# Kernel tuning notes

Hardware: AMD Instinct MI355X
Metric: run time of the kernel (lower is better)

Reference implementation:

```python
import jax, jax.numpy as jnp
import numpy as np

D_MODEL = 2048
NUM_HEADS = 16
HEAD_DIM = 128
ROPE_BASE = 10000.0
NEG_INF = -1e9


def setup_inputs() -> dict:
    key = jax.random.key(0)
    ks = jax.random.split(key, 5)
    B, S = 2, 2048
    hidden_states = jax.random.normal(ks[0], (B, S, D_MODEL), dtype=jnp.float32)
    # additive causal mask: 0 on/below diagonal, large-negative above
    causal = jnp.triu(jnp.full((S, S), NEG_INF, dtype=jnp.float32), k=1)
    attention_mask = jnp.broadcast_to(causal, (B, 1, S, S))
    position_ids = jnp.broadcast_to(jnp.arange(S, dtype=jnp.int32), (B, S))
    scale = 1.0 / np.sqrt(D_MODEL)
    Wq = jax.random.normal(ks[1], (D_MODEL, NUM_HEADS * HEAD_DIM), dtype=jnp.float32) * scale
    Wk = jax.random.normal(ks[2], (D_MODEL, NUM_HEADS * HEAD_DIM), dtype=jnp.float32) * scale
    Wv = jax.random.normal(ks[3], (D_MODEL, NUM_HEADS * HEAD_DIM), dtype=jnp.float32) * scale
    Wo = jax.random.normal(ks[4], (NUM_HEADS * HEAD_DIM, D_MODEL), dtype=jnp.float32) * scale
    return {"hidden_states": hidden_states, "attention_mask": attention_mask,
            "position_ids": position_ids, "Wq": Wq, "Wk": Wk, "Wv": Wv, "Wo": Wo}


def _rope_cos_sin(position_ids):
    # inv_freq: [head_dim/2]
    inv_freq = 1.0 / (ROPE_BASE ** (jnp.arange(0, HEAD_DIM, 2, dtype=jnp.float32) / HEAD_DIM))
    freqs = position_ids.astype(jnp.float32)[..., None] * inv_freq  # [B,S,hd/2]
    emb = jnp.concatenate([freqs, freqs], axis=-1)  # [B,S,hd]
    return jnp.cos(emb), jnp.sin(emb)


def _rotate_half(x):
    x1, x2 = jnp.split(x, 2, axis=-1)
    return jnp.concatenate([-x2, x1], axis=-1)


def reference(hidden_states, attention_mask, position_ids, Wq, Wk, Wv, Wo):
    B, S, _ = hidden_states.shape
    H, Dh = NUM_HEADS, HEAD_DIM
    q = (hidden_states @ Wq).reshape(B, S, H, Dh).transpose(0, 2, 1, 3)  # [B,H,S,Dh]
    k = (hidden_states @ Wk).reshape(B, S, H, Dh).transpose(0, 2, 1, 3)
    v = (hidden_states @ Wv).reshape(B, S, H, Dh).transpose(0, 2, 1, 3)
    cos, sin = _rope_cos_sin(position_ids)  # [B,S,Dh]
    cos = cos[:, None, :, :]  # [B,1,S,Dh]
    sin = sin[:, None, :, :]
    q = q * cos + _rotate_half(q) * sin
    k = k * cos + _rotate_half(k) * sin
    scaling = 1.0 / np.sqrt(Dh)
    scores = jnp.einsum('bhqd,bhkd->bhqk', q, k) * scaling  # [B,H,S,S]
    scores = scores + attention_mask[:, :, :, :S]
    attn = jax.nn.softmax(scores.astype(jnp.float32), axis=-1).astype(q.dtype)
    # dropout p=0.0 / eval mode -> identity
    out = jnp.einsum('bhqk,bhkd->bhqd', attn, v)  # [B,H,S,Dh]
    out = out.transpose(0, 2, 1, 3).reshape(B, S, H * Dh)
    return out @ Wo
```

## Files before the change

### kernel.cpp

```cpp
#include <hip/hip_runtime.h>

typedef __attribute__((ext_vector_type(4))) float f32x4;
typedef __attribute__((ext_vector_type(16))) float f32x16;
typedef __attribute__((ext_vector_type(8))) _Float16 f16x8;
typedef __attribute__((ext_vector_type(4))) _Float16 f16x4;

#define SEQ 2048
#define DM 2048
#define NQKV 6144

__device__ __forceinline__ void gload16(const _Float16* g, _Float16* l) {
  __builtin_amdgcn_global_load_lds(
      (const __attribute__((address_space(1))) void*)g,
      (__attribute__((address_space(3))) void*)l, 16, 0, 0);
}

__global__ __launch_bounds__(256) void cvt_x_kernel(const float* __restrict__ X,
                                                    _Float16* __restrict__ Xb, int n4) {
  int i = blockIdx.x * 256 + threadIdx.x;
  if (i < n4) {
    const float4 v = ((const float4*)X)[i];
    f16x4 o;
    o.x = (_Float16)v.x; o.y = (_Float16)v.y; o.z = (_Float16)v.z; o.w = (_Float16)v.w;
    ((f16x4*)Xb)[i] = o;
  }
}

__global__ __launch_bounds__(256) void wtrans_all_kernel(const float* __restrict__ Wq,
                                                         const float* __restrict__ Wk,
                                                         const float* __restrict__ Wv,
                                                         const float* __restrict__ Wo,
                                                         _Float16* __restrict__ Wqkvt,
                                                         _Float16* __restrict__ Wot) {
  __shared__ float tile[64][65];
  const int z = blockIdx.z;
  const float* W = (z == 0) ? Wq : (z == 1) ? Wk : (z == 2) ? Wv : Wo;
  _Float16* Wt = (z < 3) ? (Wqkvt + (size_t)z * 2048 * 2048) : Wot;
  const int n0 = blockIdx.x * 64, k0 = blockIdx.y * 64;
  const int tx = threadIdx.x & 15, ty = threadIdx.x >> 4;
#pragma unroll
  for (int i = 0; i < 4; ++i) {
    const int r = ty + i * 16;
    const float4 v = *(const float4*)&W[(size_t)(k0 + r) * 2048 + n0 + tx * 4];
    tile[r][tx * 4] = v.x; tile[r][tx * 4 + 1] = v.y;
    tile[r][tx * 4 + 2] = v.z; tile[r][tx * 4 + 3] = v.w;
  }
  __syncthreads();
  const int r = threadIdx.x >> 2, u = threadIdx.x & 3;
  _Float16 o[16];
#pragma unroll
  for (int i = 0; i < 16; ++i) o[i] = (_Float16)tile[u * 16 + i][r];
  _Float16* dst = &Wt[(size_t)(n0 + r) * 2048 + k0 + u * 16];
  *(f16x8*)&dst[0] = *(f16x8*)&o[0];
  *(f16x8*)&dst[8] = *(f16x8*)&o[8];
}

__global__ __launch_bounds__(256) void rope_table_kernel(float* __restrict__ ct,
                                                         float* __restrict__ st) {
  int i = blockIdx.x * 256 + threadIdx.x;
  int pos = i >> 6, f = i & 63;
  float inv = powf(10000.0f, -(float)f / 64.0f);
  float ang = (float)pos * inv;
  ct[i] = cosf(ang);
  st[i] = sinf(ang);
}

#define BARX()                                                          \
  do { __builtin_amdgcn_sched_barrier(0); __builtin_amdgcn_s_barrier(); \
       __builtin_amdgcn_sched_barrier(0); } while (0)
#define LGKM0X()                                                        \
  do { asm volatile("s_waitcnt lgkmcnt(0)" ::: "memory");               \
       __builtin_amdgcn_sched_barrier(0); } while (0)

template <int MODE>
__global__ __launch_bounds__(512, 2) void gemm8n_kernel(
    const _Float16* __restrict__ A, const _Float16* __restrict__ Bt,
    float* __restrict__ Cout, int M, int N, int K,
    const int* __restrict__ pos_ids, const float* __restrict__ ct,
    const float* __restrict__ st, _Float16* __restrict__ Qo,
    _Float16* __restrict__ Ko, _Float16* __restrict__ Vo) {
  __shared__ __align__(16) char smem[147456];
  _Float16* As = (_Float16*)smem;
  _Float16* Bs = (_Float16*)(smem + 98304);
  const int nwg = gridDim.x * gridDim.y;
  const int orig = blockIdx.y * gridDim.x + blockIdx.x;
  const int id = (orig & 7) * (nwg >> 3) + (orig >> 3);
  const int bx = id % gridDim.x, by = id / gridDim.x;
  const int bm = by * 256, bn = bx * 128;
  const int t = threadIdx.x, lane = t & 63, w = t >> 6;
  const int wm = w >> 2, wn = w & 3;
  const int rl = lane & 15, lr4 = lane >> 4;
  const int NKT = K >> 6;

  const int srow = t >> 3;
  const int scol = ((t & 7) ^ (srow & 7)) << 3;
  const _Float16* pA = A + (size_t)(bm + srow) * K + scol;
  const _Float16* pB = Bt + (size_t)(bn + srow) * K + scol;
  _Float16* lA = As + t * 8;
  _Float16* lB = Bs + t * 8;
  const size_t rowK64 = (size_t)64 * K;

#define STA(H, KT, SLOT)                                                   \
  { const size_t _g = (size_t)((H) * 128) * K + (size_t)(KT) * 64;         \
    gload16(pA + _g, lA + (SLOT) * 16384 + (H) * 8192);                    \
    gload16(pA + _g + rowK64, lA + (SLOT) * 16384 + (H) * 8192 + 4096); }
#define STB(KT, SLOT)                                                      \
  { const size_t _g = (size_t)(KT) * 64;                                   \
    gload16(pB + _g, lB + (SLOT) * 8192);                                  \
    gload16(pB + _g + rowK64, lB + (SLOT) * 8192 + 4096); }

  const int sw0 = (lr4 ^ (rl & 7)) << 3;
  const int sw1 = ((4 + lr4) ^ (rl & 7)) << 3;
  const int aoff = (wm * 64 + rl) * 64;
  const int boff = (wn * 32 + rl) * 64;

  f16x8 a_[4][2], b_[2][2];
  f32x4 acc[2][4][2];
#pragma unroll
  for (int qm = 0; qm < 2; ++qm)
#pragma unroll
    for (int mf = 0; mf < 4; ++mf)
#pragma unroll
      for (int nf = 0; nf < 2; ++nf) acc[qm][mf][nf] = (f32x4)0.0f;

#define LOAD_A(H, SLOT)                                                 \
  { const _Float16* _p = As + (SLOT) * 16384 + (H) * 8192 + aoff;       \
    _Pragma("unroll") for (int mf = 0; mf < 4; ++mf) {                  \
      a_[mf][0] = *(const f16x8*)&_p[mf * 1024 + sw0];                  \
      a_[mf][1] = *(const f16x8*)&_p[mf * 1024 + sw1]; } }
#define LOAD_B(SLOT)                                                    \
  { const _Float16* _p = Bs + (SLOT) * 8192 + boff;                     \
    _Pragma("unroll") for (int nf = 0; nf < 2; ++nf) {                  \
      b_[nf][0] = *(const f16x8*)&_p[nf * 1024 + sw0];                  \
      b_[nf][1] = *(const f16x8*)&_p[nf * 1024 + sw1]; } }
#define MFMA_Q(QM)                                                      \
  __builtin_amdgcn_s_setprio(1);                                        \
  _Pragma("unroll") for (int mf = 0; mf < 4; ++mf)                      \
    _Pragma("unroll") for (int nf = 0; nf < 2; ++nf) {                  \
      acc[QM][mf][nf] = __builtin_amdgcn_mfma_f32_16x16x32_f16(         \
          a_[mf][0], b_[nf][0], acc[QM][mf][nf], 0, 0, 0);              \
      acc[QM][mf][nf] = __builtin_amdgcn_mfma_f32_16x16x32_f16(         \
          a_[mf][1], b_[nf][1], acc[QM][mf][nf], 0, 0, 0); }            \
  __builtin_amdgcn_s_setprio(0);
#define VM6() asm volatile("s_waitcnt vmcnt(6)" ::: "memory")
#define VM0() asm volatile("s_waitcnt vmcnt(0)" ::: "memory")

  STA(0, 0, 0); STB(0, 0); STA(1, 0, 0);
  STA(0, 1, 1); STB(1, 1); STA(1, 1, 1);
  VM6();
  BARX();

  for (int jb = 0; jb + 4 < NKT; jb += 3) {
    LOAD_A(0, 0); LOAD_B(0); STA(0, jb + 2, 2); STB(jb + 2, 2);
    BARX(); LGKM0X(); MFMA_Q(0); BARX();
    LOAD_A(1, 0); STA(1, jb + 2, 2);
    VM6(); BARX(); LGKM0X(); MFMA_Q(1); BARX();
    LOAD_A(0, 1); LOAD_B(1); STA(0, jb + 3, 0); STB(jb + 3, 0);
    BARX(); LGKM0X(); MFMA_Q(0); BARX();
    LOAD_A(1, 1); STA(1, jb + 3, 0);
    VM6(); BARX(); LGKM0X(); MFMA_Q(1); BARX();
    LOAD_A(0, 2); LOAD_B(2); STA(0, jb + 4, 1); STB(jb + 4, 1);
    BARX(); LGKM0X(); MFMA_Q(0); BARX();
    LOAD_A(1, 2); STA(1, jb + 4, 1);
    VM6(); BARX(); LGKM0X(); MFMA_Q(1); BARX();
  }
  {
    LOAD_A(0, 0); LOAD_B(0);
    BARX(); LGKM0X(); MFMA_Q(0); BARX();
    LOAD_A(1, 0);
    VM0();
    BARX(); LGKM0X(); MFMA_Q(1); BARX();
    LOAD_A(0, 1); LOAD_B(1);
    BARX(); LGKM0X(); MFMA_Q(0); BARX();
    LOAD_A(1, 1);
    BARX(); LGKM0X(); MFMA_Q(1);
  }

  if (MODE == 0) {
#pragma unroll
    for (int qm = 0; qm < 2; ++qm)
#pragma unroll
      for (int mf = 0; mf < 4; ++mf)
#pragma unroll
        for (int nf = 0; nf < 2; ++nf) {
          const int col = bn + wn * 32 + nf * 16 + rl;
#pragma unroll
          for (int ri = 0; ri < 4; ++ri) {
            const int row = bm + qm * 128 + wm * 64 + mf * 16 + lr4 * 4 + ri;
            Cout[(size_t)row * N + col] = acc[qm][mf][nf][ri];
          }
        }
  } else {
    const int ttype = bx >> 4;
    const int hh = bx & 15;
    if (ttype == 2) {
#pragma unroll
      for (int qm = 0; qm < 2; ++qm)
#pragma unroll
        for (int mf = 0; mf < 4; ++mf)
#pragma unroll
          for (int nf = 0; nf < 2; ++nf) {
            const int d = wn * 32 + nf * 16 + rl;
            const int s0 = bm + qm * 128 + wm * 64 + mf * 16 + lr4 * 4;
            const int bb = s0 >> 11, ss = s0 & 2047;
            f16x4 v4;
#pragma unroll
            for (int ri = 0; ri < 4; ++ri) v4[ri] = (_Float16)acc[qm][mf][nf][ri];
            *(f16x4*)&Vo[((size_t)(bb * 16 + hh) * 128 + d) * SEQ + ss] = v4;
          }
    } else {
      float* cl = (float*)smem;
      LGKM0X();
      BARX();
#pragma unroll
      for (int qm = 0; qm < 2; ++qm)
#pragma unroll
        for (int mf = 0; mf < 4; ++mf)
#pragma unroll
          for (int nf = 0; nf < 2; ++nf) {
            const int col = wn * 32 + nf * 16 + rl;
            const int r0 = qm * 128 + wm * 64 + mf * 16 + lr4 * 4;
#pragma unroll
            for (int ri = 0; ri < 4; ++ri) cl[(r0 + ri) * 130 + col] = acc[qm][mf][nf][ri];
          }
      BARX();
      const int row = t >> 1, pb = (t & 1) * 32;
      const int rg = bm + row;
      const int bb = rg >> 11, ss = rg & 2047;
      const int pos = pos_ids[rg];
      const float* cp = ct + pos * 64 + pb;
      const float* sp = st + pos * 64 + pb;
      _Float16* dst = (ttype ? Ko : Qo) + ((size_t)(bb * 16 + hh) * SEQ + ss) * 128;
      const float qs = ttype ? 1.0f : 0.08838834764831845f;
      const float* crow = cl + row * 130;
      _Float16 o1[32], o2[32];
#pragma unroll
      for (int i = 0; i < 32; ++i) {
        const float x1 = crow[pb + i], x2 = crow[pb + 64 + i];
        const float c = cp[i], s = sp[i];
        o1[i] = (_Float16)((x1 * c - x2 * s) * qs);
        o2[i] = (_Float16)((x2 * c + x1 * s) * qs);
      }
#pragma unroll
      for (int i = 0; i < 4; ++i) {
        *(f16x8*)&dst[pb + i * 8] = *(f16x8*)&o1[i * 8];
        *(f16x8*)&dst[pb + 64 + i * 8] = *(f16x8*)&o2[i * 8];
      }
    }
  }
#undef STA
#undef STB
#undef LOAD_A
#undef LOAD_B
#undef MFMA_Q
#undef VM6
#undef VM0
}

__global__ __launch_bounds__(512) void attn_kernel(const _Float16* __restrict__ Q,
                                                   const _Float16* __restrict__ K,
                                                   const _Float16* __restrict__ Vt,
                                                   _Float16* __restrict__ O) {
  __shared__ __align__(16) _Float16 Ks[2][128 * 128];
  __shared__ __align__(16) _Float16 Vs[2][128 * 128];
  __shared__ __align__(16) _Float16 Ps[128 * 128];
  const int bh = blockIdx.x;
  const int pair = blockIdx.y;
  const int b = bh >> 4, h = bh & 15;
  const int t = threadIdx.x, lane = t & 63, w = t >> 6;
  const int rowgrp = w & 3, kh = w >> 2;
  const int l31 = lane & 31, l5 = lane >> 5;
  const _Float16* Qb = Q + (size_t)bh * SEQ * 128;
  const _Float16* Kb = K + (size_t)bh * SEQ * 128;
  const _Float16* Vb = Vt + (size_t)bh * 128 * SEQ;

  f16x8 onef;
#pragma unroll
  for (int i = 0; i < 8; ++i) onef[i] = (_Float16)1.0f;

  auto stage = [&](int buf, int kb) {
    const int k0 = kb * 128;
#pragma unroll
    for (int i = 0; i < 4; ++i) {
      const int c = i * 512 + t;
      const int row = c >> 4, u = c & 15;
      gload16(&Kb[(size_t)(k0 + row) * 128 + ((u ^ (row & 7)) << 3)], &Ks[buf][c * 8]);
    }
#pragma unroll
    for (int i = 0; i < 4; ++i) {
      const int c = i * 512 + t;
      const int dim = c >> 4, u = c & 15;
      gload16(&Vb[(size_t)dim * SEQ + k0 + ((u ^ (dim & 7)) << 3)], &Vs[buf][c * 8]);
    }
  };

  for (int half = 0; half < 2; ++half) {
    const int j = half ? (15 - pair) : pair;
    const int q0 = j * 128;
    const int nkb = j + 1;

    const int prow = rowgrp * 32 + l31;
    const int qrow = q0 + prow;
    f16x8 qf[8];
#pragma unroll
    for (int kc = 0; kc < 8; ++kc)
      qf[kc] = *(const f16x8*)&Qb[(size_t)qrow * 128 + kc * 16 + l5 * 8];

    f32x16 acco0 = (f32x16)0.0f, acco1 = (f32x16)0.0f, lsum = (f32x16)0.0f;

    stage(0, 0);
    for (int kb = 0; kb < nkb; ++kb) {
      const int cur = kb & 1;
      if (kb + 1 < nkb) {
        stage(cur ^ 1, kb + 1);
        asm volatile("s_waitcnt vmcnt(8)" ::: "memory");
      } else {
        asm volatile("s_waitcnt vmcnt(0)" ::: "memory");
      }
      BARX();
      const int k0 = kb * 128;
      f32x16 sacc0 = (f32x16)0.0f, sacc1 = (f32x16)0.0f;
      const int key0 = kh * 64 + l31;
      const int ksw = (l31 & 7) << 3;
#pragma unroll
      for (int kc = 0; kc < 8; ++kc) {
        const int off = kc * 16 + l5 * 8;
        sacc0 = __builtin_amdgcn_mfma_f32_32x32x16_f16(
            *(const f16x8*)&Ks[cur][key0 * 128 + (off ^ ksw)], qf[kc], sacc0, 0, 0, 0);
        sacc1 = __builtin_amdgcn_mfma_f32_32x32x16_f16(
            *(const f16x8*)&Ks[cur][(key0 + 32) * 128 + (off ^ ksw)], qf[kc], sacc1, 0, 0, 0);
      }
      const bool diag = (kb == j);
      const int rsw = (prow & 7) << 3;
#pragma unroll
      for (int kb2 = 0; kb2 < 2; ++kb2) {
        const int kbase = kh * 64 + kb2 * 32;
#pragma unroll
        for (int g = 0; g < 4; ++g) {
          f16x4 p4;
#pragma unroll
          for (int e = 0; e < 4; ++e) {
            const int reg = g * 4 + e;
            float sv = kb2 ? sacc1[reg] : sacc0[reg];
            if (diag) {
              const int key_l = kbase + g * 8 + 4 * l5 + e;
              if (k0 + key_l > q0 + prow) sv = -1e30f;
            }
            p4[e] = (_Float16)__expf(sv);
          }
          const int key4 = kbase + g * 8 + 4 * l5;
          *(f16x4*)&Ps[prow * 128 + (key4 ^ rsw)] = p4;
        }
      }
      LGKM0X();
      BARX();
      f16x8 pA[8];
#pragma unroll
      for (int kc = 0; kc < 8; ++kc)
        pA[kc] = *(const f16x8*)&Ps[prow * 128 + ((kc * 16 + l5 * 8) ^ rsw)];
#pragma unroll
      for (int kc = 0; kc < 8; ++kc)
        lsum = __builtin_amdgcn_mfma_f32_32x32x16_f16(pA[kc], onef, lsum, 0, 0, 0);
      const int d0 = kh * 64 + l31;
      const int dsw = (l31 & 7) << 3;
#pragma unroll
      for (int kc = 0; kc < 8; ++kc) {
        const int off = kc * 16 + l5 * 8;
        acco0 = __builtin_amdgcn_mfma_f32_32x32x16_f16(
            pA[kc], *(const f16x8*)&Vs[cur][d0 * 128 + (off ^ dsw)], acco0, 0, 0, 0);
        acco1 = __builtin_amdgcn_mfma_f32_32x32x16_f16(
            pA[kc], *(const f16x8*)&Vs[cur][(d0 + 32) * 128 + (off ^ dsw)], acco1, 0, 0, 0);
      }
      BARX();
    }
#pragma unroll
    for (int reg = 0; reg < 16; ++reg) {
      const int row = q0 + rowgrp * 32 + (reg & 3) + 8 * (reg >> 2) + 4 * l5;
      const float inv = 1.0f / lsum[reg];
      _Float16* orow = &O[(size_t)(b * SEQ + row) * DM + h * 128 + kh * 64 + l31];
      orow[0] = (_Float16)(acco0[reg] * inv);
      orow[32] = (_Float16)(acco1[reg] * inv);
    }
  }
}

extern "C" void kernel_launch(void* const* d_in, const int* in_sizes, int n_in,
                              void* d_out, int out_size, void* d_ws, size_t ws_size,
                              hipStream_t stream) {
  const float* hidden = (const float*)d_in[0];
  const int* pos_ids = (const int*)d_in[2];
  const float* Wq = (const float*)d_in[3];
  const float* Wk = (const float*)d_in[4];
  const float* Wv = (const float*)d_in[5];
  const float* Wo = (const float*)d_in[6];

  char* ws = (char*)d_ws;
  _Float16* Xb    = (_Float16*)(ws + 0);
  _Float16* Wqkvt = (_Float16*)(ws + 16777216);
  _Float16* Wot   = (_Float16*)(ws + 41943040);
  _Float16* Qbuf  = (_Float16*)(ws + 50331648);
  _Float16* Kbuf  = (_Float16*)(ws + 67108864);
  _Float16* Vtbuf = (_Float16*)(ws + 83886080);
  _Float16* Obuf  = (_Float16*)(ws + 100663296);
  float* ct       = (float*)(ws + 117440512);
  float* st       = (float*)(ws + 117964800);

  cvt_x_kernel<<<8192, 256, 0, stream>>>(hidden, Xb, 2097152);
  wtrans_all_kernel<<<dim3(32, 32, 4), 256, 0, stream>>>(Wq, Wk, Wv, Wo, Wqkvt, Wot);
  rope_table_kernel<<<512, 256, 0, stream>>>(ct, st);

  gemm8n_kernel<1><<<dim3(48, 16), 512, 0, stream>>>(
      Xb, Wqkvt, nullptr, 4096, 6144, 2048, pos_ids, ct, st, Qbuf, Kbuf, Vtbuf);

  attn_kernel<<<dim3(32, 8), 512, 0, stream>>>(Qbuf, Kbuf, Vtbuf, Obuf);

  gemm8n_kernel<0><<<dim3(16, 16), 512, 0, stream>>>(
      Obuf, Wot, (float*)d_out, 4096, 2048, 2048, nullptr, nullptr, nullptr,
      nullptr, nullptr, nullptr);
}
```

Measured before the change: 245.6 us.

## Share K/V tile loads across both paired causal query blocks

Each workgroup handles a pair of query blocks (j and 15-j). Before, it streamed K/V tiles separately for each block. Now it streams the K/V tiles once for the longer block and processes the shorter block's queries against the same staged tiles while they are still resident in LDS. This roughly halves the global-to-LDS K/V traffic and the pipeline prologues per workgroup. In exchange it doubles the live accumulator and Q-fragment registers, which can lower occupancy or cause spills, and it adds an extra barrier per iteration.

```diff
diff --git a/kernel.cpp b/kernel.cpp
--- a/kernel.cpp
+++ b/kernel.cpp
@@ -294,92 +294,111 @@
     }
   };
 
-  for (int half = 0; half < 2; ++half) {
-    const int j = half ? (15 - pair) : pair;
-    const int q0 = j * 128;
-    const int nkb = j + 1;
-
-    const int prow = rowgrp * 32 + l31;
-    const int qrow = q0 + prow;
-    f16x8 qf[8];
+  const int jA = pair, jB = 15 - pair;
+  const int q0A = jA * 128, q0B = jB * 128;
+  const int nkbA = jA + 1, nkbB = jB + 1;
+  const int prow = rowgrp * 32 + l31;
+  const int rsw = (prow & 7) << 3;
+
+  f16x8 qfA[8], qfB[8];
+#pragma unroll
+  for (int kc = 0; kc < 8; ++kc) {
+    qfA[kc] = *(const f16x8*)&Qb[(size_t)(q0A + prow) * 128 + kc * 16 + l5 * 8];
+    qfB[kc] = *(const f16x8*)&Qb[(size_t)(q0B + prow) * 128 + kc * 16 + l5 * 8];
+  }
+
+  f32x16 accA0 = (f32x16)0.0f, accA1 = (f32x16)0.0f, lsumA = (f32x16)0.0f;
+  f32x16 accB0 = (f32x16)0.0f, accB1 = (f32x16)0.0f, lsumB = (f32x16)0.0f;
+
+  auto process = [&](const f16x8* qf, f32x16& a0, f32x16& a1, f32x16& ls,
+                     bool diag, int q0loc, int k0, int cur) {
+    f32x16 s0 = (f32x16)0.0f, s1 = (f32x16)0.0f;
+    const int key0 = kh * 64 + l31;
+    const int ksw = (l31 & 7) << 3;
+#pragma unroll
+    for (int kc = 0; kc < 8; ++kc) {
+      const int off = kc * 16 + l5 * 8;
+      s0 = __builtin_amdgcn_mfma_f32_32x32x16_f16(
+          *(const f16x8*)&Ks[cur][key0 * 128 + (off ^ ksw)], qf[kc], s0, 0, 0, 0);
+      s1 = __builtin_amdgcn_mfma_f32_32x32x16_f16(
+          *(const f16x8*)&Ks[cur][(key0 + 32) * 128 + (off ^ ksw)], qf[kc], s1, 0, 0, 0);
+    }
+#pragma unroll
+    for (int kb2 = 0; kb2 < 2; ++kb2) {
+      const int kbase = kh * 64 + kb2 * 32;
+#pragma unroll
+      for (int g = 0; g < 4; ++g) {
+        f16x4 p4;
+#pragma unroll
+        for (int e = 0; e < 4; ++e) {
+          const int reg = g * 4 + e;
+          float sv = kb2 ? s1[reg] : s0[reg];
+          if (diag) {
+            const int key_l = kbase + g * 8 + 4 * l5 + e;
+            if (k0 + key_l > q0loc + prow) sv = -1e30f;
+          }
+          p4[e] = (_Float16)__expf(sv);
+        }
+        const int key4 = kbase + g * 8 + 4 * l5;
+        *(f16x4*)&Ps[prow * 128 + (key4 ^ rsw)] = p4;
+      }
+    }
+    LGKM0X();
+    BARX();
+    f16x8 pA[8];
 #pragma unroll
     for (int kc = 0; kc < 8; ++kc)
-      qf[kc] = *(const f16x8*)&Qb[(size_t)qrow * 128 + kc * 16 + l5 * 8];
-
-    f32x16 acco0 = (f32x16)0.0f, acco1 = (f32x16)0.0f, lsum = (f32x16)0.0f;
-
-    stage(0, 0);
-    for (int kb = 0; kb < nkb; ++kb) {
-      const int cur = kb & 1;
-      if (kb + 1 < nkb) {
-        stage(cur ^ 1, kb + 1);
-        asm volatile("s_waitcnt vmcnt(8)" ::: "memory");
-      } else {
-        asm volatile("s_waitcnt vmcnt(0)" ::: "memory");
-      }
+      pA[kc] = *(const f16x8*)&Ps[prow * 128 + ((kc * 16 + l5 * 8) ^ rsw)];
+#pragma unroll
+    for (int kc = 0; kc < 8; ++kc)
+      ls = __builtin_amdgcn_mfma_f32_32x32x16_f16(pA[kc], onef, ls, 0, 0, 0);
+    const int d0 = kh * 64 + l31;
+    const int dsw = (l31 & 7) << 3;
+#pragma unroll
+    for (int kc = 0; kc < 8; ++kc) {
+      const int off = kc * 16 + l5 * 8;
+      a0 = __builtin_amdgcn_mfma_f32_32x32x16_f16(
+          pA[kc], *(const f16x8*)&Vs[cur][d0 * 128 + (off ^ dsw)], a0, 0, 0, 0);
+      a1 = __builtin_amdgcn_mfma_f32_32x32x16_f16(
+          pA[kc], *(const f16x8*)&Vs[cur][(d0 + 32) * 128 + (off ^ dsw)], a1, 0, 0, 0);
+    }
+  };
+
+  stage(0, 0);
+  for (int kb = 0; kb < nkbB; ++kb) {
+    const int cur = kb & 1;
+    if (kb + 1 < nkbB) {
+      stage(cur ^ 1, kb + 1);
+      asm volatile("s_waitcnt vmcnt(8)" ::: "memory");
+    } else {
+      asm volatile("s_waitcnt vmcnt(0)" ::: "memory");
+    }
+    BARX();
+    const int k0 = kb * 128;
+    process(qfB, accB0, accB1, lsumB, kb == jB, q0B, k0, cur);
+    if (kb < nkbA) {
       BARX();
-      const int k0 = kb * 128;
-      f32x16 sacc0 = (f32x16)0.0f, sacc1 = (f32x16)0.0f;
-      const int key0 = kh * 64 + l31;
-      const int ksw = (l31 & 7) << 3;
-#pragma unroll
-      for (int kc = 0; kc < 8; ++kc) {
-        const int off = kc * 16 + l5 * 8;
-        sacc0 = __builtin_amdgcn_mfma_f32_32x32x16_f16(
-            *(const f16x8*)&Ks[cur][key0 * 128 + (off ^ ksw)], qf[kc], sacc0, 0, 0, 0);
-        sacc1 = __builtin_amdgcn_mfma_f32_32x32x16_f16(
-            *(const f16x8*)&Ks[cur][(key0 + 32) * 128 + (off ^ ksw)], qf[kc], sacc1, 0, 0, 0);
-      }
-      const bool diag = (kb == j);
-      const int rsw = (prow & 7) << 3;
-#pragma unroll
-      for (int kb2 = 0; kb2 < 2; ++kb2) {
-        const int kbase = kh * 64 + kb2 * 32;
-#pragma unroll
-        for (int g = 0; g < 4; ++g) {
-          f16x4 p4;
-#pragma unroll
-          for (int e = 0; e < 4; ++e) {
-            const int reg = g * 4 + e;
-            float sv = kb2 ? sacc1[reg] : sacc0[reg];
-            if (diag) {
-              const int key_l = kbase + g * 8 + 4 * l5 + e;
-              if (k0 + key_l > q0 + prow) sv = -1e30f;
-            }
-            p4[e] = (_Float16)__expf(sv);
-          }
-          const int key4 = kbase + g * 8 + 4 * l5;
-          *(f16x4*)&Ps[prow * 128 + (key4 ^ rsw)] = p4;
-        }
-      }
-      LGKM0X();
-      BARX();
-      f16x8 pA[8];
-#pragma unroll
-      for (int kc = 0; kc < 8; ++kc)
-        pA[kc] = *(const f16x8*)&Ps[prow * 128 + ((kc * 16 + l5 * 8) ^ rsw)];
-#pragma unroll
-      for (int kc = 0; kc < 8; ++kc)
-        lsum = __builtin_amdgcn_mfma_f32_32x32x16_f16(pA[kc], onef, lsum, 0, 0, 0);
-      const int d0 = kh * 64 + l31;
-      const int dsw = (l31 & 7) << 3;
-#pragma unroll
-      for (int kc = 0; kc < 8; ++kc) {
-        const int off = kc * 16 + l5 * 8;
-        acco0 = __builtin_amdgcn_mfma_f32_32x32x16_f16(
-            pA[kc], *(const f16x8*)&Vs[cur][d0 * 128 + (off ^ dsw)], acco0, 0, 0, 0);
-        acco1 = __builtin_amdgcn_mfma_f32_32x32x16_f16(
-            pA[kc], *(const f16x8*)&Vs[cur][(d0 + 32) * 128 + (off ^ dsw)], acco1, 0, 0, 0);
-      }
-      BARX();
-    }
-#pragma unroll
-    for (int reg = 0; reg < 16; ++reg) {
-      const int row = q0 + rowgrp * 32 + (reg & 3) + 8 * (reg >> 2) + 4 * l5;
-      const float inv = 1.0f / lsum[reg];
-      _Float16* orow = &O[(size_t)(b * SEQ + row) * DM + h * 128 + kh * 64 + l31];
-      orow[0] = (_Float16)(acco0[reg] * inv);
-      orow[32] = (_Float16)(acco1[reg] * inv);
+      process(qfA, accA0, accA1, lsumA, kb == jA, q0A, k0, cur);
+    }
+    BARX();
+  }
+
+#pragma unroll
+  for (int reg = 0; reg < 16; ++reg) {
+    const int rowoff = rowgrp * 32 + (reg & 3) + 8 * (reg >> 2) + 4 * l5;
+    {
+      const float inv = 1.0f / lsumA[reg];
+      _Float16* orow =
+          &O[(size_t)(b * SEQ + q0A + rowoff) * DM + h * 128 + kh * 64 + l31];
+      orow[0] = (_Float16)(accA0[reg] * inv);
+      orow[32] = (_Float16)(accA1[reg] * inv);
+    }
+    {
+      const float inv = 1.0f / lsumB[reg];
+      _Float16* orow =
+          &O[(size_t)(b * SEQ + q0B + rowoff) * DM + h * 128 + kh * 64 + l31];
+      orow[0] = (_Float16)(accB0[reg] * inv);
+      orow[32] = (_Float16)(accB1[reg] * inv);
     }
   }
 }
```

After: 280.6 us. +14.3%, slower.
